# Performance work log

Measured on AMD Instinct MI355X. Metric: run time of the kernel, lower is better.

The kernel has to match this reference:

```python
import jax, jax.numpy as jnp
import numpy as np
import math

B, S, DIM = 2, 2048, 1024
H, D = 16, 64  # num_head, head_dim; H*D == DIM

def setup_inputs() -> dict:
    key = jax.random.key(0)
    ks = jax.random.split(key, 10)
    s = 0.02
    return {
        "X": jax.random.normal(ks[0], (B, S, DIM), dtype=jnp.float32),
        "mask": jnp.ones((B, S), dtype=jnp.float32),
        "Wq": jax.random.normal(ks[1], (DIM, H * D), dtype=jnp.float32) * s,
        "bq": jnp.zeros((H * D,), dtype=jnp.float32),
        "Wk": jax.random.normal(ks[2], (DIM, H * D), dtype=jnp.float32) * s,
        "bk": jnp.zeros((H * D,), dtype=jnp.float32),
        "Wv": jax.random.normal(ks[3], (DIM, H * D), dtype=jnp.float32) * s,
        "bv": jnp.zeros((H * D,), dtype=jnp.float32),
        "Wo": jax.random.normal(ks[4], (H * D, DIM), dtype=jnp.float32) * s,
        "bo": jnp.zeros((DIM,), dtype=jnp.float32),
    }

def _split_heads(x):
    # [B, S, H*D] -> [B, H, S, D]
    b, s, _ = x.shape
    return x.reshape(b, s, H, D).transpose(0, 2, 1, 3)

def reference(X, mask, Wq, bq, Wk, bk, Wv, bv, Wo, bo):
    Q = _split_heads(X @ Wq + bq)
    K = _split_heads(X @ Wk + bk)
    V = _split_heads(X @ Wv + bv)
    # scaled dot-product attention with additive mask penalty
    dot = jnp.einsum('bhqd,bhkd->bhqk', Q, K) / math.sqrt(D)
    dot = dot - 1e6 * (1.0 - mask[:, None, None, :])
    attn = jax.nn.softmax(dot, axis=-1)
    ctx = jnp.einsum('bhqk,bhkd->bhqd', attn, V)
    # combine heads: [B, H, S, D] -> [B, S, H*D]
    ctx = ctx.transpose(0, 2, 1, 3).reshape(B, S, H * D)
    return ctx @ Wo + bo
```

## Files before the change

### kernel.cpp

```cpp
#include <hip/hip_runtime.h>
#include <cstdint>
#include <cstddef>

typedef __attribute__((ext_vector_type(8))) _Float16 f16x8;
typedef __attribute__((ext_vector_type(4))) _Float16 f16x4;
typedef __attribute__((ext_vector_type(4))) float f32x4;

#define MFMA_16x16x32(a, b, c) __builtin_amdgcn_mfma_f32_16x16x32_f16((a), (b), (c), 0, 0, 0)

static constexpr int kB = 2, kS = 2048, kDim = 1024, kH = 16, kD = 64;
static constexpr int kM = kB * kS;
static constexpr float kQScale = 0.125f * 1.44269504088896340736f;
static constexpr float kPenC = 1.44269504088896340736e6f;

__device__ __forceinline__ void wg_barrier_lds() {
  asm volatile("s_waitcnt lgkmcnt(0)" ::: "memory");
  __builtin_amdgcn_s_barrier();
}

__global__ void cvt_f32_to_f16(const float* __restrict__ in, _Float16* __restrict__ out, int n8) {
  int i = blockIdx.x * blockDim.x + threadIdx.x;
  if (i >= n8) return;
  const float4* p = (const float4*)in + (size_t)i * 2;
  float4 a = p[0], b = p[1];
  f16x8 h;
  h[0] = (_Float16)a.x; h[1] = (_Float16)a.y; h[2] = (_Float16)a.z; h[3] = (_Float16)a.w;
  h[4] = (_Float16)b.x; h[5] = (_Float16)b.y; h[6] = (_Float16)b.z; h[7] = (_Float16)b.w;
  ((f16x8*)out)[i] = h;
}

__global__ void transpose_cvt_w(const float* __restrict__ w0, const float* __restrict__ w1,
                                const float* __restrict__ w2, const float* __restrict__ w3,
                                _Float16* __restrict__ o0, _Float16* __restrict__ o1,
                                _Float16* __restrict__ o2, _Float16* __restrict__ o3) {
  const float* w; _Float16* o;
  switch (blockIdx.z) {
    case 0: w = w0; o = o0; break;
    case 1: w = w1; o = o1; break;
    case 2: w = w2; o = o2; break;
    default: w = w3; o = o3; break;
  }
  __shared__ alignas(16) _Float16 tile[64][72];
  const int kt = blockIdx.x * 64;
  const int nt = blockIdx.y * 64;
  const int tr = threadIdx.x >> 4;
  const int tc = threadIdx.x & 15;
#pragma unroll
  for (int rr = 0; rr < 4; ++rr) {
    int r = rr * 16 + tr;
    float4 v = *(const float4*)&w[(size_t)(kt + r) * kDim + nt + tc * 4];
    f16x4 hv;
    hv[0] = (_Float16)v.x; hv[1] = (_Float16)v.y; hv[2] = (_Float16)v.z; hv[3] = (_Float16)v.w;
    *(f16x4*)&tile[r][tc * 4] = hv;
  }
  __syncthreads();
#pragma unroll
  for (int rr = 0; rr < 4; ++rr) {
    int nl = rr * 16 + tr;
    f16x4 hv;
    hv[0] = tile[tc * 4 + 0][nl];
    hv[1] = tile[tc * 4 + 1][nl];
    hv[2] = tile[tc * 4 + 2][nl];
    hv[3] = tile[tc * 4 + 3][nl];
    *(f16x4*)&o[(size_t)(nt + nl) * kDim + kt + tc * 4] = hv;
  }
}

__global__ __launch_bounds__(256, 2) void gemm_qkv(
    const _Float16* __restrict__ A,
    const _Float16* __restrict__ wt0, const _Float16* __restrict__ wt1, const _Float16* __restrict__ wt2,
    const float* __restrict__ bias0, const float* __restrict__ bias1, const float* __restrict__ bias2,
    _Float16* __restrict__ oq, _Float16* __restrict__ ok, _Float16* __restrict__ ov) {
  const _Float16* Bt; const float* bias; _Float16* out;
  switch (blockIdx.z) {
    case 0: Bt = wt0; bias = bias0; out = oq; break;
    case 1: Bt = wt1; bias = bias1; out = ok; break;
    default: Bt = wt2; bias = bias2; out = ov; break;
  }
  __shared__ alignas(16) _Float16 As[2][128 * 72];
  __shared__ alignas(16) _Float16 Bs[2][128 * 72];
  const int tid = threadIdx.x;
  const int lane = tid & 63;
  const int wave = tid >> 6;
  const int wm = wave & 1, wn = wave >> 1;
  const int l15 = lane & 15, quad = lane >> 4;
  const int m0 = blockIdx.x * 128, n0 = blockIdx.y * 128;

  const int srow = tid >> 3;
  const int skc = (tid & 7) * 8;

  f32x4 acc[4][4] = {};
  f16x8 ra[4], rb[4];

#pragma unroll
  for (int i = 0; i < 4; ++i) {
    int row = srow + 32 * i;
    ra[i] = *(const f16x8*)&A[(size_t)(m0 + row) * kDim + skc];
    rb[i] = *(const f16x8*)&Bt[(size_t)(n0 + row) * kDim + skc];
  }
#pragma unroll
  for (int i = 0; i < 4; ++i) {
    int row = srow + 32 * i;
    *(f16x8*)&As[0][row * 72 + skc] = ra[i];
    *(f16x8*)&Bs[0][row * 72 + skc] = rb[i];
  }

  for (int kt = 0; kt < 16; ++kt) {
    const int cur = kt & 1;
    if (kt + 1 < 16) {
      int k0 = (kt + 1) * 64;
#pragma unroll
      for (int i = 0; i < 4; ++i) {
        int row = srow + 32 * i;
        ra[i] = *(const f16x8*)&A[(size_t)(m0 + row) * kDim + k0 + skc];
        rb[i] = *(const f16x8*)&Bt[(size_t)(n0 + row) * kDim + k0 + skc];
      }
    }
    wg_barrier_lds();
#pragma unroll
    for (int kk = 0; kk < 2; ++kk) {
      f16x8 af[4], bf[4];
#pragma unroll
      for (int t = 0; t < 4; ++t) af[t] = *(const f16x8*)&As[cur][(wm * 64 + t * 16 + l15) * 72 + kk * 32 + quad * 8];
#pragma unroll
      for (int t = 0; t < 4; ++t) bf[t] = *(const f16x8*)&Bs[cur][(wn * 64 + t * 16 + l15) * 72 + kk * 32 + quad * 8];
      __builtin_amdgcn_s_setprio(1);
#pragma unroll
      for (int i = 0; i < 4; ++i)
#pragma unroll
        for (int j = 0; j < 4; ++j)
          acc[i][j] = MFMA_16x16x32(af[i], bf[j], acc[i][j]);
      __builtin_amdgcn_s_setprio(0);
    }
    if (kt + 1 < 16) {
#pragma unroll
      for (int i = 0; i < 4; ++i) {
        int row = srow + 32 * i;
        *(f16x8*)&As[cur ^ 1][row * 72 + skc] = ra[i];
        *(f16x8*)&Bs[cur ^ 1][row * 72 + skc] = rb[i];
      }
    }
  }

  const int mbase = m0 + wm * 64 + quad * 4;
  const int nbase = n0 + wn * 64 + l15;
  if (blockIdx.z == 2) {
#pragma unroll
    for (int j = 0; j < 4; ++j) {
      int n = nbase + j * 16;
      float bv = bias[n];
      int h = n >> 6, d = n & 63;
#pragma unroll
      for (int i = 0; i < 4; ++i) {
        int m = mbase + i * 16;
        int b = m >> 11, s = m & (kS - 1);
        f16x4 hv;
#pragma unroll
        for (int r = 0; r < 4; ++r) hv[r] = (_Float16)(acc[i][j][r] + bv);
        *(f16x4*)&out[((size_t)((b * kH + h) * kD + d)) * kS + s] = hv;
      }
    }
  } else {
    const float osc = (blockIdx.z == 0) ? kQScale : 1.0f;
#pragma unroll
    for (int j = 0; j < 4; ++j) {
      int n = nbase + j * 16;
      float bv = bias[n];
      int h = n >> 6, d = n & 63;
#pragma unroll
      for (int i = 0; i < 4; ++i) {
        int mrow = mbase + i * 16;
#pragma unroll
        for (int r = 0; r < 4; ++r) {
          int m = mrow + r;
          int b = m >> 11, s = m & (kS - 1);
          out[(size_t)(((b * kH + h) * kS) + s) * kD + d] = (_Float16)((acc[i][j][r] + bv) * osc);
        }
      }
    }
  }
}

__global__ __launch_bounds__(256, 2) void attn(
    const _Float16* __restrict__ Q, const _Float16* __restrict__ K,
    const _Float16* __restrict__ V, const float* __restrict__ mask,
    _Float16* __restrict__ ctx) {
  const int id = blockIdx.x;
  const int logical = (id & 7) * 64 + (id >> 3);
  const int bh = logical >> 4;
  const int qblk = logical & 15;
  const int b = bh >> 4;
  const int q0 = qblk * 128;
  const int tid = threadIdx.x, lane = tid & 63, wave = tid >> 6;
  const int l15 = lane & 15, quad = lane >> 4;

  __shared__ alignas(16) _Float16 Ks[128 * 72];
  __shared__ alignas(16) _Float16 Vs[64 * 136];
  __shared__ alignas(16) _Float16 Pt[4][32 * 136];
  __shared__ alignas(16) float pens[kS];

  const _Float16* Qh = Q + (size_t)bh * kS * kD;
  const _Float16* Kh = K + (size_t)bh * kS * kD;
  const _Float16* Vh = V + (size_t)bh * kS * kD;

#pragma unroll
  for (int i = 0; i < 2; ++i) {
    float4 mv4 = *(const float4*)&mask[(size_t)b * kS + tid * 8 + i * 4];
    float4 pv;
    pv.x = (mv4.x - 1.0f) * kPenC;
    pv.y = (mv4.y - 1.0f) * kPenC;
    pv.z = (mv4.z - 1.0f) * kPenC;
    pv.w = (mv4.w - 1.0f) * kPenC;
    *(float4*)&pens[tid * 8 + i * 4] = pv;
  }

  f16x8 qf[2][2];
#pragma unroll
  for (int t = 0; t < 2; ++t) {
    int qrow = q0 + wave * 32 + t * 16 + l15;
#pragma unroll
    for (int kk = 0; kk < 2; ++kk)
      qf[t][kk] = *(const f16x8*)&Qh[(size_t)qrow * kD + kk * 32 + quad * 8];
  }

  f32x4 o_acc[2][4] = {};
  float l_part[2] = {0.0f, 0.0f};

  const int srow = tid >> 3;
  const int skc = (tid & 7) * 8;
  const int vrow = tid >> 4;
  const int vcol = (tid & 15) * 8;

  f16x8 kreg[4], vreg[4];
#pragma unroll
  for (int i = 0; i < 4; ++i)
    kreg[i] = *(const f16x8*)&Kh[(size_t)(srow + 32 * i) * kD + skc];
#pragma unroll
  for (int i = 0; i < 4; ++i)
    vreg[i] = *(const f16x8*)&Vh[(size_t)(vrow + 16 * i) * kS + vcol];

  for (int it = 0; it < 16; ++it) {
    const int kb = it * 128;
    wg_barrier_lds();
#pragma unroll
    for (int i = 0; i < 4; ++i)
      *(f16x8*)&Ks[(srow + 32 * i) * 72 + skc] = kreg[i];
#pragma unroll
    for (int i = 0; i < 4; ++i)
      *(f16x8*)&Vs[(vrow + 16 * i) * 136 + vcol] = vreg[i];
    if (it + 1 < 16) {
#pragma unroll
      for (int i = 0; i < 4; ++i)
        kreg[i] = *(const f16x8*)&Kh[(size_t)(kb + 128 + srow + 32 * i) * kD + skc];
#pragma unroll
      for (int i = 0; i < 4; ++i)
        vreg[i] = *(const f16x8*)&Vh[(size_t)(vrow + 16 * i) * kS + kb + 128 + vcol];
    }
    wg_barrier_lds();

#pragma unroll
    for (int colt = 0; colt < 8; ++colt) {
      f16x8 kf0 = *(const f16x8*)&Ks[(colt * 16 + l15) * 72 + quad * 8];
      f16x8 kf1 = *(const f16x8*)&Ks[(colt * 16 + l15) * 72 + 32 + quad * 8];
      f32x4 s0 = {}, s1 = {};
      __builtin_amdgcn_s_setprio(1);
      s0 = MFMA_16x16x32(kf0, qf[0][0], s0);
      s0 = MFMA_16x16x32(kf1, qf[0][1], s0);
      s1 = MFMA_16x16x32(kf0, qf[1][0], s1);
      s1 = MFMA_16x16x32(kf1, qf[1][1], s1);
      __builtin_amdgcn_s_setprio(0);
      f32x4 pn = *(const f32x4*)&pens[kb + colt * 16 + quad * 4];
      f16x4 ph0, ph1;
#pragma unroll
      for (int r = 0; r < 4; ++r) {
        float p0 = __builtin_exp2f(s0[r] + pn[r]);
        float p1 = __builtin_exp2f(s1[r] + pn[r]);
        l_part[0] += p0;
        l_part[1] += p1;
        ph0[r] = (_Float16)p0;
        ph1[r] = (_Float16)p1;
      }
      *(f16x4*)&Pt[wave][(l15) * 136 + colt * 16 + quad * 4] = ph0;
      *(f16x4*)&Pt[wave][(16 + l15) * 136 + colt * 16 + quad * 4] = ph1;
    }

#pragma unroll
    for (int ks = 0; ks < 4; ++ks) {
      f16x8 pf0 = *(const f16x8*)&Pt[wave][(l15) * 136 + ks * 32 + quad * 8];
      f16x8 pf1 = *(const f16x8*)&Pt[wave][(16 + l15) * 136 + ks * 32 + quad * 8];
      f16x8 vf0 = *(const f16x8*)&Vs[(0 * 16 + l15) * 136 + ks * 32 + quad * 8];
      f16x8 vf1 = *(const f16x8*)&Vs[(1 * 16 + l15) * 136 + ks * 32 + quad * 8];
      f16x8 vf2 = *(const f16x8*)&Vs[(2 * 16 + l15) * 136 + ks * 32 + quad * 8];
      f16x8 vf3 = *(const f16x8*)&Vs[(3 * 16 + l15) * 136 + ks * 32 + quad * 8];
      __builtin_amdgcn_s_setprio(1);
      o_acc[0][0] = MFMA_16x16x32(vf0, pf0, o_acc[0][0]);
      o_acc[1][0] = MFMA_16x16x32(vf0, pf1, o_acc[1][0]);
      o_acc[0][1] = MFMA_16x16x32(vf1, pf0, o_acc[0][1]);
      o_acc[1][1] = MFMA_16x16x32(vf1, pf1, o_acc[1][1]);
      o_acc[0][2] = MFMA_16x16x32(vf2, pf0, o_acc[0][2]);
      o_acc[1][2] = MFMA_16x16x32(vf2, pf1, o_acc[1][2]);
      o_acc[0][3] = MFMA_16x16x32(vf3, pf0, o_acc[0][3]);
      o_acc[1][3] = MFMA_16x16x32(vf3, pf1, o_acc[1][3]);
      __builtin_amdgcn_s_setprio(0);
    }
  }

  const int h = bh & 15;
#pragma unroll
  for (int t = 0; t < 2; ++t) {
    float lsum = l_part[t];
    lsum += __shfl_xor(lsum, 16, 64);
    lsum += __shfl_xor(lsum, 32, 64);
    float inv = 1.0f / lsum;
    int q = q0 + wave * 32 + t * 16 + l15;
#pragma unroll
    for (int c = 0; c < 4; ++c) {
      f16x4 oh;
#pragma unroll
      for (int r = 0; r < 4; ++r) oh[r] = (_Float16)(o_acc[t][c][r] * inv);
      *(f16x4*)&ctx[((size_t)(b * kS + q)) * kDim + h * kD + c * 16 + quad * 4] = oh;
    }
  }
}

__global__ __launch_bounds__(256, 2) void gemm_out(
    const _Float16* __restrict__ A, const _Float16* __restrict__ Bt,
    const float* __restrict__ bias, float* __restrict__ out) {
  __shared__ alignas(16) _Float16 As[2][128 * 72];
  __shared__ alignas(16) _Float16 Bs[2][128 * 72];
  const int tid = threadIdx.x;
  const int lane = tid & 63;
  const int wave = tid >> 6;
  const int wm = wave & 1, wn = wave >> 1;
  const int l15 = lane & 15, quad = lane >> 4;
  const int m0 = blockIdx.x * 128, n0 = blockIdx.y * 128;

  const int srow = tid >> 3;
  const int skc = (tid & 7) * 8;

  f32x4 acc[4][4] = {};
  f16x8 ra[4], rb[4];

#pragma unroll
  for (int i = 0; i < 4; ++i) {
    int row = srow + 32 * i;
    ra[i] = *(const f16x8*)&A[(size_t)(m0 + row) * kDim + skc];
    rb[i] = *(const f16x8*)&Bt[(size_t)(n0 + row) * kDim + skc];
  }
#pragma unroll
  for (int i = 0; i < 4; ++i) {
    int row = srow + 32 * i;
    *(f16x8*)&As[0][row * 72 + skc] = ra[i];
    *(f16x8*)&Bs[0][row * 72 + skc] = rb[i];
  }

  for (int kt = 0; kt < 16; ++kt) {
    const int cur = kt & 1;
    if (kt + 1 < 16) {
      int k0 = (kt + 1) * 64;
#pragma unroll
      for (int i = 0; i < 4; ++i) {
        int row = srow + 32 * i;
        ra[i] = *(const f16x8*)&A[(size_t)(m0 + row) * kDim + k0 + skc];
        rb[i] = *(const f16x8*)&Bt[(size_t)(n0 + row) * kDim + k0 + skc];
      }
    }
    wg_barrier_lds();
#pragma unroll
    for (int kk = 0; kk < 2; ++kk) {
      f16x8 af[4], bf[4];
#pragma unroll
      for (int t = 0; t < 4; ++t) af[t] = *(const f16x8*)&As[cur][(wm * 64 + t * 16 + l15) * 72 + kk * 32 + quad * 8];
#pragma unroll
      for (int t = 0; t < 4; ++t) bf[t] = *(const f16x8*)&Bs[cur][(wn * 64 + t * 16 + l15) * 72 + kk * 32 + quad * 8];
      __builtin_amdgcn_s_setprio(1);
#pragma unroll
      for (int i = 0; i < 4; ++i)
#pragma unroll
        for (int j = 0; j < 4; ++j)
          acc[i][j] = MFMA_16x16x32(af[i], bf[j], acc[i][j]);
      __builtin_amdgcn_s_setprio(0);
    }
    if (kt + 1 < 16) {
#pragma unroll
      for (int i = 0; i < 4; ++i) {
        int row = srow + 32 * i;
        *(f16x8*)&As[cur ^ 1][row * 72 + skc] = ra[i];
        *(f16x8*)&Bs[cur ^ 1][row * 72 + skc] = rb[i];
      }
    }
  }

  const int mbase = m0 + wm * 64 + quad * 4;
  const int nbase = n0 + wn * 64 + l15;
#pragma unroll
  for (int j = 0; j < 4; ++j) {
    int n = nbase + j * 16;
    float bv = bias[n];
#pragma unroll
    for (int i = 0; i < 4; ++i) {
      int mrow = mbase + i * 16;
#pragma unroll
      for (int r = 0; r < 4; ++r)
        out[(size_t)(mrow + r) * kDim + n] = acc[i][j][r] + bv;
    }
  }
}

extern "C" void kernel_launch(void* const* d_in, const int* in_sizes, int n_in,
                              void* d_out, int out_size, void* d_ws, size_t ws_size,
                              hipStream_t stream) {
  (void)in_sizes; (void)n_in; (void)out_size; (void)ws_size;
  const float* X    = (const float*)d_in[0];
  const float* mask = (const float*)d_in[1];
  const float* Wq   = (const float*)d_in[2];
  const float* bq   = (const float*)d_in[3];
  const float* Wk   = (const float*)d_in[4];
  const float* bk   = (const float*)d_in[5];
  const float* Wv   = (const float*)d_in[6];
  const float* bv   = (const float*)d_in[7];
  const float* Wo   = (const float*)d_in[8];
  const float* bo   = (const float*)d_in[9];
  float* out = (float*)d_out;

  char* ws = (char*)d_ws;
  _Float16* Xh   = (_Float16*)(ws);
  _Float16* Wqt  = (_Float16*)(ws + ((size_t)8  << 20));
  _Float16* Wkt  = (_Float16*)(ws + ((size_t)10 << 20));
  _Float16* Wvt  = (_Float16*)(ws + ((size_t)12 << 20));
  _Float16* Wot  = (_Float16*)(ws + ((size_t)14 << 20));
  _Float16* Qh   = (_Float16*)(ws + ((size_t)16 << 20));
  _Float16* Kh   = (_Float16*)(ws + ((size_t)24 << 20));
  _Float16* Vh   = (_Float16*)(ws + ((size_t)32 << 20));
  _Float16* Ch   = (_Float16*)(ws + ((size_t)40 << 20));

  cvt_f32_to_f16<<<dim3(kM * kDim / 8 / 256), dim3(256), 0, stream>>>(X, Xh, kM * kDim / 8);
  transpose_cvt_w<<<dim3(16, 16, 4), dim3(256), 0, stream>>>(Wq, Wk, Wv, Wo, Wqt, Wkt, Wvt, Wot);
  gemm_qkv<<<dim3(32, 8, 3), dim3(256), 0, stream>>>(Xh, Wqt, Wkt, Wvt, bq, bk, bv, Qh, Kh, Vh);
  attn<<<dim3(512), dim3(256), 0, stream>>>(Qh, Kh, Vh, mask, Ch);
  gemm_out<<<dim3(32, 8), dim3(256), 0, stream>>>(Ch, Wot, bo, out);
}
```

Baseline: 209.5 us.

## Halve attention and output GEMM tiles to double grid size and occupancy

The attention kernel now processes 64 query rows per block, with 16 per wave, and 64-key tiles, so the grid grows from 512 to 1024 blocks and launch bounds allow 4 blocks per CU. The row-sum is now computed by an extra MFMA against a ones vector instead of scalar accumulation plus shuffles. The output GEMM uses 64-row M tiles, so it launches twice as many blocks. The aim is to fill all CUs on a 256-CU part and hide latency through occupancy. The cost is less reuse of each K/V load per block, twice as many barrier iterations, and an extra MFMA per step.

```diff
diff --git a/kernel.cpp b/kernel.cpp
--- a/kernel.cpp
+++ b/kernel.cpp
@@ -181,22 +181,22 @@
   }
 }
 
-__global__ __launch_bounds__(256, 2) void attn(
+__global__ __launch_bounds__(256, 4) void attn(
     const _Float16* __restrict__ Q, const _Float16* __restrict__ K,
     const _Float16* __restrict__ V, const float* __restrict__ mask,
     _Float16* __restrict__ ctx) {
   const int id = blockIdx.x;
-  const int logical = (id & 7) * 64 + (id >> 3);
-  const int bh = logical >> 4;
-  const int qblk = logical & 15;
+  const int logical = (id & 7) * 128 + (id >> 3);
+  const int bh = logical >> 5;
+  const int qblk = logical & 31;
   const int b = bh >> 4;
-  const int q0 = qblk * 128;
+  const int q0 = qblk * 64;
   const int tid = threadIdx.x, lane = tid & 63, wave = tid >> 6;
   const int l15 = lane & 15, quad = lane >> 4;
 
-  __shared__ alignas(16) _Float16 Ks[128 * 72];
-  __shared__ alignas(16) _Float16 Vs[64 * 136];
-  __shared__ alignas(16) _Float16 Pt[4][32 * 136];
+  __shared__ alignas(16) _Float16 Ks[64 * 72];
+  __shared__ alignas(16) _Float16 Vs[64 * 72];
+  __shared__ alignas(16) _Float16 Pt[4][16 * 72];
   __shared__ alignas(16) float pens[kS];
 
   const _Float16* Qh = Q + (size_t)bh * kS * kD;
@@ -214,168 +214,150 @@
     *(float4*)&pens[tid * 8 + i * 4] = pv;
   }
 
-  f16x8 qf[2][2];
-#pragma unroll
-  for (int t = 0; t < 2; ++t) {
-    int qrow = q0 + wave * 32 + t * 16 + l15;
+  f16x8 qf[2];
+  {
+    int qrow = q0 + wave * 16 + l15;
 #pragma unroll
     for (int kk = 0; kk < 2; ++kk)
-      qf[t][kk] = *(const f16x8*)&Qh[(size_t)qrow * kD + kk * 32 + quad * 8];
-  }
-
-  f32x4 o_acc[2][4] = {};
-  float l_part[2] = {0.0f, 0.0f};
+      qf[kk] = *(const f16x8*)&Qh[(size_t)qrow * kD + kk * 32 + quad * 8];
+  }
+
+  f16x8 ones;
+#pragma unroll
+  for (int i = 0; i < 8; ++i) ones[i] = (_Float16)1.0f;
+
+  f32x4 o_acc[4] = {};
+  f32x4 l_acc = {};
 
   const int srow = tid >> 3;
   const int skc = (tid & 7) * 8;
-  const int vrow = tid >> 4;
-  const int vcol = (tid & 15) * 8;
-
-  f16x8 kreg[4], vreg[4];
-#pragma unroll
-  for (int i = 0; i < 4; ++i)
+
+  f16x8 kreg[2], vreg[2];
+#pragma unroll
+  for (int i = 0; i < 2; ++i)
     kreg[i] = *(const f16x8*)&Kh[(size_t)(srow + 32 * i) * kD + skc];
 #pragma unroll
-  for (int i = 0; i < 4; ++i)
-    vreg[i] = *(const f16x8*)&Vh[(size_t)(vrow + 16 * i) * kS + vcol];
-
-  for (int it = 0; it < 16; ++it) {
-    const int kb = it * 128;
+  for (int i = 0; i < 2; ++i)
+    vreg[i] = *(const f16x8*)&Vh[(size_t)(srow + 32 * i) * kS + skc];
+
+  for (int it = 0; it < 32; ++it) {
+    const int kb = it * 64;
     wg_barrier_lds();
 #pragma unroll
-    for (int i = 0; i < 4; ++i)
+    for (int i = 0; i < 2; ++i)
       *(f16x8*)&Ks[(srow + 32 * i) * 72 + skc] = kreg[i];
 #pragma unroll
-    for (int i = 0; i < 4; ++i)
-      *(f16x8*)&Vs[(vrow + 16 * i) * 136 + vcol] = vreg[i];
-    if (it + 1 < 16) {
-#pragma unroll
-      for (int i = 0; i < 4; ++i)
-        kreg[i] = *(const f16x8*)&Kh[(size_t)(kb + 128 + srow + 32 * i) * kD + skc];
-#pragma unroll
-      for (int i = 0; i < 4; ++i)
-        vreg[i] = *(const f16x8*)&Vh[(size_t)(vrow + 16 * i) * kS + kb + 128 + vcol];
+    for (int i = 0; i < 2; ++i)
+      *(f16x8*)&Vs[(srow + 32 * i) * 72 + skc] = vreg[i];
+    if (it + 1 < 32) {
+#pragma unroll
+      for (int i = 0; i < 2; ++i)
+        kreg[i] = *(const f16x8*)&Kh[(size_t)(kb + 64 + srow + 32 * i) * kD + skc];
+#pragma unroll
+      for (int i = 0; i < 2; ++i)
+        vreg[i] = *(const f16x8*)&Vh[(size_t)(srow + 32 * i) * kS + kb + 64 + skc];
     }
     wg_barrier_lds();
 
 #pragma unroll
-    for (int colt = 0; colt < 8; ++colt) {
+    for (int colt = 0; colt < 4; ++colt) {
       f16x8 kf0 = *(const f16x8*)&Ks[(colt * 16 + l15) * 72 + quad * 8];
       f16x8 kf1 = *(const f16x8*)&Ks[(colt * 16 + l15) * 72 + 32 + quad * 8];
-      f32x4 s0 = {}, s1 = {};
+      f32x4 s = {};
       __builtin_amdgcn_s_setprio(1);
-      s0 = MFMA_16x16x32(kf0, qf[0][0], s0);
-      s0 = MFMA_16x16x32(kf1, qf[0][1], s0);
-      s1 = MFMA_16x16x32(kf0, qf[1][0], s1);
-      s1 = MFMA_16x16x32(kf1, qf[1][1], s1);
+      s = MFMA_16x16x32(kf0, qf[0], s);
+      s = MFMA_16x16x32(kf1, qf[1], s);
       __builtin_amdgcn_s_setprio(0);
       f32x4 pn = *(const f32x4*)&pens[kb + colt * 16 + quad * 4];
-      f16x4 ph0, ph1;
-#pragma unroll
-      for (int r = 0; r < 4; ++r) {
-        float p0 = __builtin_exp2f(s0[r] + pn[r]);
-        float p1 = __builtin_exp2f(s1[r] + pn[r]);
-        l_part[0] += p0;
-        l_part[1] += p1;
-        ph0[r] = (_Float16)p0;
-        ph1[r] = (_Float16)p1;
-      }
-      *(f16x4*)&Pt[wave][(l15) * 136 + colt * 16 + quad * 4] = ph0;
-      *(f16x4*)&Pt[wave][(16 + l15) * 136 + colt * 16 + quad * 4] = ph1;
-    }
-
-#pragma unroll
-    for (int ks = 0; ks < 4; ++ks) {
-      f16x8 pf0 = *(const f16x8*)&Pt[wave][(l15) * 136 + ks * 32 + quad * 8];
-      f16x8 pf1 = *(const f16x8*)&Pt[wave][(16 + l15) * 136 + ks * 32 + quad * 8];
-      f16x8 vf0 = *(const f16x8*)&Vs[(0 * 16 + l15) * 136 + ks * 32 + quad * 8];
-      f16x8 vf1 = *(const f16x8*)&Vs[(1 * 16 + l15) * 136 + ks * 32 + quad * 8];
-      f16x8 vf2 = *(const f16x8*)&Vs[(2 * 16 + l15) * 136 + ks * 32 + quad * 8];
-      f16x8 vf3 = *(const f16x8*)&Vs[(3 * 16 + l15) * 136 + ks * 32 + quad * 8];
+      f16x4 ph;
+#pragma unroll
+      for (int r = 0; r < 4; ++r)
+        ph[r] = (_Float16)__builtin_exp2f(s[r] + pn[r]);
+      *(f16x4*)&Pt[wave][l15 * 72 + colt * 16 + quad * 4] = ph;
+    }
+
+#pragma unroll
+    for (int ks = 0; ks < 2; ++ks) {
+      f16x8 pf = *(const f16x8*)&Pt[wave][l15 * 72 + ks * 32 + quad * 8];
+      f16x8 vf0 = *(const f16x8*)&Vs[(0 * 16 + l15) * 72 + ks * 32 + quad * 8];
+      f16x8 vf1 = *(const f16x8*)&Vs[(1 * 16 + l15) * 72 + ks * 32 + quad * 8];
+      f16x8 vf2 = *(const f16x8*)&Vs[(2 * 16 + l15) * 72 + ks * 32 + quad * 8];
+      f16x8 vf3 = *(const f16x8*)&Vs[(3 * 16 + l15) * 72 + ks * 32 + quad * 8];
       __builtin_amdgcn_s_setprio(1);
-      o_acc[0][0] = MFMA_16x16x32(vf0, pf0, o_acc[0][0]);
-      o_acc[1][0] = MFMA_16x16x32(vf0, pf1, o_acc[1][0]);
-      o_acc[0][1] = MFMA_16x16x32(vf1, pf0, o_acc[0][1]);
-      o_acc[1][1] = MFMA_16x16x32(vf1, pf1, o_acc[1][1]);
-      o_acc[0][2] = MFMA_16x16x32(vf2, pf0, o_acc[0][2]);
-      o_acc[1][2] = MFMA_16x16x32(vf2, pf1, o_acc[1][2]);
-      o_acc[0][3] = MFMA_16x16x32(vf3, pf0, o_acc[0][3]);
-      o_acc[1][3] = MFMA_16x16x32(vf3, pf1, o_acc[1][3]);
+      o_acc[0] = MFMA_16x16x32(vf0, pf, o_acc[0]);
+      o_acc[1] = MFMA_16x16x32(vf1, pf, o_acc[1]);
+      o_acc[2] = MFMA_16x16x32(vf2, pf, o_acc[2]);
+      o_acc[3] = MFMA_16x16x32(vf3, pf, o_acc[3]);
+      l_acc = MFMA_16x16x32(ones, pf, l_acc);
       __builtin_amdgcn_s_setprio(0);
     }
   }
 
   const int h = bh & 15;
-#pragma unroll
-  for (int t = 0; t < 2; ++t) {
-    float lsum = l_part[t];
-    lsum += __shfl_xor(lsum, 16, 64);
-    lsum += __shfl_xor(lsum, 32, 64);
-    float inv = 1.0f / lsum;
-    int q = q0 + wave * 32 + t * 16 + l15;
-#pragma unroll
-    for (int c = 0; c < 4; ++c) {
-      f16x4 oh;
-#pragma unroll
-      for (int r = 0; r < 4; ++r) oh[r] = (_Float16)(o_acc[t][c][r] * inv);
-      *(f16x4*)&ctx[((size_t)(b * kS + q)) * kDim + h * kD + c * 16 + quad * 4] = oh;
-    }
+  const float inv = 1.0f / l_acc[0];
+  const int q = q0 + wave * 16 + l15;
+#pragma unroll
+  for (int c = 0; c < 4; ++c) {
+    f16x4 oh;
+#pragma unroll
+    for (int r = 0; r < 4; ++r) oh[r] = (_Float16)(o_acc[c][r] * inv);
+    *(f16x4*)&ctx[((size_t)(b * kS + q)) * kDim + h * kD + c * 16 + quad * 4] = oh;
   }
 }
 
 __global__ __launch_bounds__(256, 2) void gemm_out(
     const _Float16* __restrict__ A, const _Float16* __restrict__ Bt,
     const float* __restrict__ bias, float* __restrict__ out) {
-  __shared__ alignas(16) _Float16 As[2][128 * 72];
+  __shared__ alignas(16) _Float16 As[2][64 * 72];
   __shared__ alignas(16) _Float16 Bs[2][128 * 72];
   const int tid = threadIdx.x;
   const int lane = tid & 63;
   const int wave = tid >> 6;
   const int wm = wave & 1, wn = wave >> 1;
   const int l15 = lane & 15, quad = lane >> 4;
-  const int m0 = blockIdx.x * 128, n0 = blockIdx.y * 128;
+  const int m0 = blockIdx.x * 64, n0 = blockIdx.y * 128;
 
   const int srow = tid >> 3;
   const int skc = (tid & 7) * 8;
 
-  f32x4 acc[4][4] = {};
-  f16x8 ra[4], rb[4];
-
-#pragma unroll
-  for (int i = 0; i < 4; ++i) {
-    int row = srow + 32 * i;
-    ra[i] = *(const f16x8*)&A[(size_t)(m0 + row) * kDim + skc];
-    rb[i] = *(const f16x8*)&Bt[(size_t)(n0 + row) * kDim + skc];
-  }
-#pragma unroll
-  for (int i = 0; i < 4; ++i) {
-    int row = srow + 32 * i;
-    *(f16x8*)&As[0][row * 72 + skc] = ra[i];
-    *(f16x8*)&Bs[0][row * 72 + skc] = rb[i];
-  }
+  f32x4 acc[2][4] = {};
+  f16x8 ra[2], rb[4];
+
+#pragma unroll
+  for (int i = 0; i < 2; ++i)
+    ra[i] = *(const f16x8*)&A[(size_t)(m0 + srow + 32 * i) * kDim + skc];
+#pragma unroll
+  for (int i = 0; i < 4; ++i)
+    rb[i] = *(const f16x8*)&Bt[(size_t)(n0 + srow + 32 * i) * kDim + skc];
+#pragma unroll
+  for (int i = 0; i < 2; ++i)
+    *(f16x8*)&As[0][(srow + 32 * i) * 72 + skc] = ra[i];
+#pragma unroll
+  for (int i = 0; i < 4; ++i)
+    *(f16x8*)&Bs[0][(srow + 32 * i) * 72 + skc] = rb[i];
 
   for (int kt = 0; kt < 16; ++kt) {
     const int cur = kt & 1;
     if (kt + 1 < 16) {
       int k0 = (kt + 1) * 64;
 #pragma unroll
-      for (int i = 0; i < 4; ++i) {
-        int row = srow + 32 * i;
-        ra[i] = *(const f16x8*)&A[(size_t)(m0 + row) * kDim + k0 + skc];
-        rb[i] = *(const f16x8*)&Bt[(size_t)(n0 + row) * kDim + k0 + skc];
-      }
+      for (int i = 0; i < 2; ++i)
+        ra[i] = *(const f16x8*)&A[(size_t)(m0 + srow + 32 * i) * kDim + k0 + skc];
+#pragma unroll
+      for (int i = 0; i < 4; ++i)
+        rb[i] = *(const f16x8*)&Bt[(size_t)(n0 + srow + 32 * i) * kDim + k0 + skc];
     }
     wg_barrier_lds();
 #pragma unroll
     for (int kk = 0; kk < 2; ++kk) {
-      f16x8 af[4], bf[4];
-#pragma unroll
-      for (int t = 0; t < 4; ++t) af[t] = *(const f16x8*)&As[cur][(wm * 64 + t * 16 + l15) * 72 + kk * 32 + quad * 8];
+      f16x8 af[2], bf[4];
+#pragma unroll
+      for (int t = 0; t < 2; ++t) af[t] = *(const f16x8*)&As[cur][(wm * 32 + t * 16 + l15) * 72 + kk * 32 + quad * 8];
 #pragma unroll
       for (int t = 0; t < 4; ++t) bf[t] = *(const f16x8*)&Bs[cur][(wn * 64 + t * 16 + l15) * 72 + kk * 32 + quad * 8];
       __builtin_amdgcn_s_setprio(1);
 #pragma unroll
-      for (int i = 0; i < 4; ++i)
+      for (int i = 0; i < 2; ++i)
 #pragma unroll
         for (int j = 0; j < 4; ++j)
           acc[i][j] = MFMA_16x16x32(af[i], bf[j], acc[i][j]);
@@ -383,22 +365,22 @@
     }
     if (kt + 1 < 16) {
 #pragma unroll
-      for (int i = 0; i < 4; ++i) {
-        int row = srow + 32 * i;
-        *(f16x8*)&As[cur ^ 1][row * 72 + skc] = ra[i];
-        *(f16x8*)&Bs[cur ^ 1][row * 72 + skc] = rb[i];
-      }
-    }
-  }
-
-  const int mbase = m0 + wm * 64 + quad * 4;
+      for (int i = 0; i < 2; ++i)
+        *(f16x8*)&As[cur ^ 1][(srow + 32 * i) * 72 + skc] = ra[i];
+#pragma unroll
+      for (int i = 0; i < 4; ++i)
+        *(f16x8*)&Bs[cur ^ 1][(srow + 32 * i) * 72 + skc] = rb[i];
+    }
+  }
+
+  const int mbase = m0 + wm * 32 + quad * 4;
   const int nbase = n0 + wn * 64 + l15;
 #pragma unroll
   for (int j = 0; j < 4; ++j) {
     int n = nbase + j * 16;
     float bv = bias[n];
 #pragma unroll
-    for (int i = 0; i < 4; ++i) {
+    for (int i = 0; i < 2; ++i) {
       int mrow = mbase + i * 16;
 #pragma unroll
       for (int r = 0; r < 4; ++r)
@@ -437,6 +419,6 @@
   cvt_f32_to_f16<<<dim3(kM * kDim / 8 / 256), dim3(256), 0, stream>>>(X, Xh, kM * kDim / 8);
   transpose_cvt_w<<<dim3(16, 16, 4), dim3(256), 0, stream>>>(Wq, Wk, Wv, Wo, Wqt, Wkt, Wvt, Wot);
   gemm_qkv<<<dim3(32, 8, 3), dim3(256), 0, stream>>>(Xh, Wqt, Wkt, Wvt, bq, bk, bv, Qh, Kh, Vh);
-  attn<<<dim3(512), dim3(256), 0, stream>>>(Qh, Kh, Vh, mask, Ch);
-  gemm_out<<<dim3(32, 8), dim3(256), 0, stream>>>(Ch, Wot, bo, out);
-}
+  attn<<<dim3(1024), dim3(256), 0, stream>>>(Qh, Kh, Vh, mask, Ch);
+  gemm_out<<<dim3(64, 8), dim3(256), 0, stream>>>(Ch, Wot, bo, out);
+}
```

Measured after the change: 213.6 us. Within noise of the previous version (+1.9%).
